# Optimization experiments

Hardware: AMD Instinct MI355X
Metric: run time of the kernel (lower is better)

Reference implementation:

```python
import jax, jax.numpy as jnp
import numpy as np

C = 256
RATE_CHOICE = [32, 64, 96, 128, 160, 192, 224, 256]
RATE_NUM = len(RATE_CHOICE)
MAX_RATE = max(RATE_CHOICE)
B, H, W = 16, 16, 16


def setup_inputs() -> dict:
    key = jax.random.key(0)
    k_x, k_idx, k_w = jax.random.split(key, 3)
    x = jax.random.normal(k_x, (B, C, H, W), dtype=jnp.float32)
    indexes = jax.random.randint(k_idx, (B * H * W,), 0, RATE_NUM, dtype=jnp.int64)
    # xavier_normal over (fan_in=C*MAX_RATE? torch 3D: fan_in=C*MAX_RATE, fan_out=RATE_NUM*MAX_RATE) -> use gain std
    std = float(np.sqrt(2.0 / (C + MAX_RATE)))
    weight = jax.random.normal(k_w, (RATE_NUM, C, MAX_RATE), dtype=jnp.float32) * std
    bias = jnp.zeros((RATE_NUM, MAX_RATE), dtype=jnp.float32)
    rate_choice_tensor = jnp.asarray(RATE_CHOICE, dtype=jnp.int32)
    return {"x": x, "indexes": indexes, "weight": weight, "bias": bias,
            "rate_choice_tensor": rate_choice_tensor}


def reference(x, indexes, weight, bias, rate_choice_tensor):
    Bv, Cv, Hv, Wv = x.shape
    L = Hv * Wv
    R = weight.shape[-1]
    # x: [B,C,H,W] -> [B,L,C]
    x_blc = x.reshape(Bv, Cv, L).transpose(0, 2, 1)
    # per-token gathered weights/bias
    w = weight[indexes].reshape(Bv, L, Cv, R)      # [B,L,C,R]
    b = bias[indexes].reshape(Bv, L, R)            # [B,L,R]
    # rate mask: arange(R) < rate_choice[idx]
    rc = rate_choice_tensor[indexes].reshape(Bv, L, 1)
    mask = (jnp.arange(R, dtype=rc.dtype)[None, None, :] < rc).astype(x.dtype)  # [B,L,R]
    # batched per-token matvec + bias, then mask
    y = (jnp.einsum('blc,blcr->blr', x_blc, w) + b) * mask
    x_masked = y.reshape(Bv, Hv, Wv, R).transpose(0, 3, 1, 2)     # [B,R,H,W]
    mask_bchw = mask.reshape(Bv, Hv, Wv, R).transpose(0, 3, 1, 2)
    return (x_masked, mask_bchw)
```

## Files before the change

### kernel.cpp

```cpp
#include <hip/hip_runtime.h>

#define WS_BUCKET 1024
#define WS_XT     262144
#define WS_YT     4456448
#define WS_NEED   8650752

__global__ __launch_bounds__(256) void bucket_kernel(const int* __restrict__ idx,
                                                     int* __restrict__ counts,
                                                     int* __restrict__ bucket) {
  __shared__ int lcount[8];
  __shared__ int lbase[8];
  const int tid = threadIdx.x;
  const int t = (blockIdx.x << 8) + tid;
  if (tid < 8) lcount[tid] = 0;
  __syncthreads();
  const int g = idx[t];
  const int lpos = atomicAdd(&lcount[g], 1);
  __syncthreads();
  if (tid < 8) lbase[tid] = atomicAdd(&counts[tid], lcount[tid]);
  __syncthreads();
  bucket[(g << 12) + lbase[g] + lpos] = t;
}

__global__ __launch_bounds__(256) void xpose_kernel(const float* __restrict__ x,
                                                    float* __restrict__ xT) {
  __shared__ float tile[32][33];
  const int b = blockIdx.x;
  const int c0 = (blockIdx.y >> 3) << 5;
  const int l0 = (blockIdx.y & 7) << 5;
  const int j = threadIdx.x & 31;
  const int i = threadIdx.x >> 5;
#pragma unroll
  for (int ii = 0; ii < 4; ++ii) {
    const int c = c0 + (ii << 3) + i;
    tile[(ii << 3) + i][j] = x[(b << 16) + (c << 8) + l0 + j];
  }
  __syncthreads();
#pragma unroll
  for (int ii = 0; ii < 4; ++ii) {
    const int l = l0 + (ii << 3) + i;
    xT[(((b << 8) + l) << 8) + c0 + j] = tile[j][(ii << 3) + i];
  }
}

__global__ __launch_bounds__(256) void gemv_kernel(const float* __restrict__ xT,
                                                   const float* __restrict__ W,
                                                   const float* __restrict__ bias,
                                                   const int* __restrict__ counts,
                                                   const int* __restrict__ bucket,
                                                   float* __restrict__ yT) {
  const int g = blockIdx.x;
  const int n = counts[g];
  const int t0 = blockIdx.y << 3;
  if (t0 >= n) return;
  const int nt = min(8, n - t0);
  const int r = threadIdx.x;

  __shared__ float xs[8][256];
  __shared__ int toks[8];
  if (r < 8) toks[r] = (r < nt) ? bucket[(g << 12) + t0 + r] : bucket[(g << 12) + t0];
  __syncthreads();
#pragma unroll
  for (int t = 0; t < 8; ++t) xs[t][r] = xT[(toks[t] << 8) + r];
  __syncthreads();

  float acc[8];
  const float brv = bias[(g << 8) + r];
#pragma unroll
  for (int t = 0; t < 8; ++t) acc[t] = brv;

  const float* w = W + (g << 16) + r;
  for (int c4 = 0; c4 < 64; ++c4) {
    const float w0 = w[((c4 << 2) + 0) << 8];
    const float w1 = w[((c4 << 2) + 1) << 8];
    const float w2 = w[((c4 << 2) + 2) << 8];
    const float w3 = w[((c4 << 2) + 3) << 8];
#pragma unroll
    for (int t = 0; t < 8; ++t) {
      const float4 xv = *reinterpret_cast<const float4*>(&xs[t][c4 << 2]);
      acc[t] += xv.x * w0 + xv.y * w1 + xv.z * w2 + xv.w * w3;
    }
  }

  for (int t = 0; t < nt; ++t) yT[(toks[t] << 8) + r] = acc[t];
}

__global__ __launch_bounds__(256) void out_kernel(const float* __restrict__ yT,
                                                  const int* __restrict__ idx,
                                                  const int* __restrict__ rate,
                                                  float* __restrict__ out) {
  __shared__ float tile[32][33];
  __shared__ int rcl[32];
  const int b = blockIdx.x;
  const int r0 = (blockIdx.y >> 3) << 5;
  const int l0 = (blockIdx.y & 7) << 5;
  const int j = threadIdx.x & 31;
  const int i = threadIdx.x >> 5;
#pragma unroll
  for (int ii = 0; ii < 4; ++ii) {
    const int l = l0 + (ii << 3) + i;
    tile[(ii << 3) + i][j] = yT[(((b << 8) + l) << 8) + r0 + j];
  }
  if (threadIdx.x < 32) rcl[threadIdx.x] = rate[idx[(b << 8) + l0 + threadIdx.x]];
  __syncthreads();
#pragma unroll
  for (int ii = 0; ii < 4; ++ii) {
    const int r = r0 + (ii << 3) + i;
    const float m = (r < rcl[j]) ? 1.0f : 0.0f;
    const int o = (b << 16) + (r << 8) + l0 + j;
    out[o] = tile[j][(ii << 3) + i] * m;
    out[(1 << 20) + o] = m;
  }
}

__global__ __launch_bounds__(256) void rate_tok_kernel(
    const float* __restrict__ x, const int* __restrict__ indexes,
    const float* __restrict__ W, const float* __restrict__ bias,
    const int* __restrict__ rate, float* __restrict__ out) {
  const int t = blockIdx.x;
  const int b = t >> 8;
  const int l = t & 255;
  const int r = threadIdx.x;
  __shared__ float xs[256];
  xs[r] = x[(b << 16) + (r << 8) + l];
  const int g = indexes[t];
  const int rc = rate[g];
  __syncthreads();
  const float* w = W + (g << 16) + r;
  float acc = bias[(g << 8) + r];
#pragma unroll 8
  for (int c = 0; c < 256; ++c) acc += xs[c] * w[c << 8];
  const float m = (r < rc) ? 1.0f : 0.0f;
  const int o = (b << 16) + (r << 8) + l;
  out[o] = acc * m;
  out[(1 << 20) + o] = m;
}

extern "C" void kernel_launch(void* const* d_in, const int* in_sizes, int n_in,
                              void* d_out, int out_size, void* d_ws, size_t ws_size,
                              hipStream_t stream) {
  const float* x    = (const float*)d_in[0];
  const int*   idx  = (const int*)d_in[1];
  const float* W    = (const float*)d_in[2];
  const float* bias = (const float*)d_in[3];
  const int*   rate = (const int*)d_in[4];
  float* out = (float*)d_out;

  if (ws_size >= (size_t)WS_NEED) {
    int*   counts = (int*)d_ws;
    int*   bucket = (int*)((char*)d_ws + WS_BUCKET);
    float* xT     = (float*)((char*)d_ws + WS_XT);
    float* yT     = (float*)((char*)d_ws + WS_YT);
    hipMemsetAsync(counts, 0, 8 * sizeof(int), stream);
    bucket_kernel<<<dim3(16), dim3(256), 0, stream>>>(idx, counts, bucket);
    xpose_kernel<<<dim3(16, 64), dim3(256), 0, stream>>>(x, xT);
    gemv_kernel<<<dim3(8, 512), dim3(256), 0, stream>>>(xT, W, bias, counts, bucket, yT);
    out_kernel<<<dim3(16, 64), dim3(256), 0, stream>>>(yT, idx, rate, out);
  } else {
    rate_tok_kernel<<<dim3(4096), dim3(256), 0, stream>>>(x, idx, W, bias, rate, out);
  }
}
```

Baseline: 97.34 us.

## Retile gemv: 16 tokens per block, 4x4 register tile per thread with float4 loads

The gemv kernel now handles 16 tokens per block instead of 8. Each wavefront owns 4 tokens and each lane computes 4 adjacent output rates, loading weights and x as float4. This halves the number of blocks that re-read the same weight matrix and raises the number of FMAs per loaded weight value. The cost is more registers per thread and fewer blocks, which may lower occupancy and parallelism.

```diff
diff --git a/kernel.cpp b/kernel.cpp
--- a/kernel.cpp
+++ b/kernel.cpp
@@ -51,38 +51,59 @@
                                                    float* __restrict__ yT) {
   const int g = blockIdx.x;
   const int n = counts[g];
-  const int t0 = blockIdx.y << 3;
+  const int t0 = blockIdx.y << 4;
   if (t0 >= n) return;
-  const int nt = min(8, n - t0);
-  const int r = threadIdx.x;
+  const int nt = min(16, n - t0);
+  const int tid = threadIdx.x;
+  const int lane = tid & 63;
+  const int wid = tid >> 6;
 
-  __shared__ float xs[8][256];
-  __shared__ int toks[8];
-  if (r < 8) toks[r] = (r < nt) ? bucket[(g << 12) + t0 + r] : bucket[(g << 12) + t0];
+  __shared__ float xs[16][256];
+  __shared__ int toks[16];
+  if (tid < 16) toks[tid] = bucket[(g << 12) + min(t0 + tid, n - 1)];
   __syncthreads();
 #pragma unroll
-  for (int t = 0; t < 8; ++t) xs[t][r] = xT[(toks[t] << 8) + r];
+  for (int tt = 0; tt < 4; ++tt) {
+    const int t = (wid << 2) + tt;
+    const float4* src = reinterpret_cast<const float4*>(xT + (toks[t] << 8));
+    reinterpret_cast<float4*>(&xs[t][0])[lane] = src[lane];
+  }
   __syncthreads();
 
-  float acc[8];
-  const float brv = bias[(g << 8) + r];
+  const int r0 = lane << 2;
+  float acc[4][4];
+  const float4 bv = *reinterpret_cast<const float4*>(bias + (g << 8) + r0);
 #pragma unroll
-  for (int t = 0; t < 8; ++t) acc[t] = brv;
+  for (int tt = 0; tt < 4; ++tt) {
+    acc[tt][0] = bv.x; acc[tt][1] = bv.y; acc[tt][2] = bv.z; acc[tt][3] = bv.w;
+  }
 
-  const float* w = W + (g << 16) + r;
-  for (int c4 = 0; c4 < 64; ++c4) {
-    const float w0 = w[((c4 << 2) + 0) << 8];
-    const float w1 = w[((c4 << 2) + 1) << 8];
-    const float w2 = w[((c4 << 2) + 2) << 8];
-    const float w3 = w[((c4 << 2) + 3) << 8];
+  const float* wp = W + (g << 16) + r0;
+#pragma unroll 2
+  for (int c = 0; c < 256; c += 4) {
+    const float4 w0 = *reinterpret_cast<const float4*>(wp + ((c + 0) << 8));
+    const float4 w1 = *reinterpret_cast<const float4*>(wp + ((c + 1) << 8));
+    const float4 w2 = *reinterpret_cast<const float4*>(wp + ((c + 2) << 8));
+    const float4 w3 = *reinterpret_cast<const float4*>(wp + ((c + 3) << 8));
 #pragma unroll
-    for (int t = 0; t < 8; ++t) {
-      const float4 xv = *reinterpret_cast<const float4*>(&xs[t][c4 << 2]);
-      acc[t] += xv.x * w0 + xv.y * w1 + xv.z * w2 + xv.w * w3;
+    for (int tt = 0; tt < 4; ++tt) {
+      const float4 xv = *reinterpret_cast<const float4*>(&xs[(wid << 2) + tt][c]);
+      acc[tt][0] += xv.x * w0.x + xv.y * w1.x + xv.z * w2.x + xv.w * w3.x;
+      acc[tt][1] += xv.x * w0.y + xv.y * w1.y + xv.z * w2.y + xv.w * w3.y;
+      acc[tt][2] += xv.x * w0.z + xv.y * w1.z + xv.z * w2.z + xv.w * w3.z;
+      acc[tt][3] += xv.x * w0.w + xv.y * w1.w + xv.z * w2.w + xv.w * w3.w;
     }
   }
 
-  for (int t = 0; t < nt; ++t) yT[(toks[t] << 8) + r] = acc[t];
+#pragma unroll
+  for (int tt = 0; tt < 4; ++tt) {
+    const int t = (wid << 2) + tt;
+    if (t < nt) {
+      float4 v;
+      v.x = acc[tt][0]; v.y = acc[tt][1]; v.z = acc[tt][2]; v.w = acc[tt][3];
+      *reinterpret_cast<float4*>(yT + (toks[t] << 8) + r0) = v;
+    }
+  }
 }
 
 __global__ __launch_bounds__(256) void out_kernel(const float* __restrict__ yT,
@@ -154,7 +175,7 @@
     hipMemsetAsync(counts, 0, 8 * sizeof(int), stream);
     bucket_kernel<<<dim3(16), dim3(256), 0, stream>>>(idx, counts, bucket);
     xpose_kernel<<<dim3(16, 64), dim3(256), 0, stream>>>(x, xT);
-    gemv_kernel<<<dim3(8, 512), dim3(256), 0, stream>>>(xT, W, bias, counts, bucket, yT);
+    gemv_kernel<<<dim3(8, 256), dim3(256), 0, stream>>>(xT, W, bias, counts, bucket, yT);
     out_kernel<<<dim3(16, 64), dim3(256), 0, stream>>>(yT, idx, rate, out);
   } else {
     rate_tok_kernel<<<dim3(4096), dim3(256), 0, stream>>>(x, idx, W, bias, rate, out);
```

Result: slower. 114.2 us (+17.3%).
